# Optimization experiments

Hardware: AMD Instinct MI355X
Metric: run time of the kernel (lower is better)

## Reference

```python
import jax, jax.numpy as jnp
import numpy as np

NUM_HEADS = 16
D_MODEL = 1024
HEAD_DIM = D_MODEL // NUM_HEADS
EMB = 1024
B, L = 2, 2048


def setup_inputs() -> dict:
    key = jax.random.key(0)
    k1, k2, k3 = jax.random.split(key, 3)
    scale_in = 1.0 / np.sqrt(EMB)
    scale_out = 1.0 / np.sqrt(D_MODEL)
    return {
        "x": jax.random.normal(k1, (B, L, EMB), dtype=jnp.float32),
        "W_qkv": jax.random.normal(k2, (EMB, 3 * D_MODEL), dtype=jnp.float32) * scale_in,
        "b_qkv": jnp.zeros((3 * D_MODEL,), dtype=jnp.float32),
        "W_out": jax.random.normal(k3, (D_MODEL, EMB), dtype=jnp.float32) * scale_out,
        "b_out": jnp.zeros((EMB,), dtype=jnp.float32),
    }


def reference(x, W_qkv, b_qkv, W_out, b_out):
    Bn, Ln, _ = x.shape
    qkv = x @ W_qkv + b_qkv  # [B, L, 3*d_model]
    q = qkv[:, :, :D_MODEL].reshape(Bn, Ln, NUM_HEADS, HEAD_DIM)
    k = qkv[:, :, D_MODEL:2 * D_MODEL].reshape(Bn, Ln, NUM_HEADS, HEAD_DIM)
    v = qkv[:, :, 2 * D_MODEL:].reshape(Bn, Ln, NUM_HEADS, HEAD_DIM)
    scores = jnp.einsum('bqhd,bkhd->bhqk', q, k)  # [B, H, L, L]
    attn = jax.nn.softmax(scores / jnp.sqrt(jnp.float32(HEAD_DIM)), axis=-1)
    out = jnp.einsum('bhqk,bkhd->bqhd', attn, v).reshape(Bn, Ln, D_MODEL)
    return out @ W_out + b_out
```

## Files before the change

kernel.cpp:

```cpp
#include <hip/hip_runtime.h>
#include <stdint.h>

#define B_   2
#define L_   2048
#define H_   16
#define D_   64
#define EMB_ 1024
#define DM_  1024
#define N3_  3072
#define TOK_ 4096

typedef unsigned short u16;
typedef unsigned int u32;
typedef __attribute__((ext_vector_type(4))) float f32x4;
typedef __attribute__((ext_vector_type(8))) short s16x8;
typedef __attribute__((ext_vector_type(4))) u32 u32x4;
typedef __attribute__((ext_vector_type(2))) u32 u32x2;
typedef __attribute__((ext_vector_type(4))) u16 u16x4;

#define MFMA(a,b,c) __builtin_amdgcn_mfma_f32_16x16x32_bf16(a,b,c,0,0,0)

#define AS1 __attribute__((address_space(1)))
#define AS3 __attribute__((address_space(3)))
#define GLLDS(g, l) __builtin_amdgcn_global_load_lds( \
    (const AS1 u32*)(const void*)(g), (AS3 u32*)(void*)(l), 16, 0, 0)

#define QSCALE 0.18033688011f

static __device__ __forceinline__ u16 f2bf(float f) {
  u32 u = __builtin_bit_cast(u32, f);
  u = (u + 0x7fffu + ((u >> 16) & 1u)) >> 16;
  return (u16)u;
}

static __device__ __forceinline__ u32 pack2bf(float a, float b) {
#if __has_builtin(__builtin_amdgcn_cvt_pk_bf16_f32)
  auto v = __builtin_amdgcn_cvt_pk_bf16_f32(a, b);
  return __builtin_bit_cast(u32, v);
#else
  return (u32)f2bf(a) | ((u32)f2bf(b) << 16);
#endif
}

static __device__ __forceinline__ float fexp2(float x) {
#if __has_builtin(__builtin_amdgcn_exp2f)
  return __builtin_amdgcn_exp2f(x);
#else
  float r;
  asm("v_exp_f32 %0, %1" : "=v"(r) : "v"(x));
  return r;
#endif
}

__global__ __launch_bounds__(256) void k_prep(
    const float* __restrict__ x,   u16* __restrict__ xb,
    const float* __restrict__ Wq,  u16* __restrict__ wqT,
    const float* __restrict__ Wo,  u16* __restrict__ woT)
{
  const int blk = blockIdx.x, tid = threadIdx.x;
  if (blk < 4096) {
    int i = (blk * 256 + tid) * 4;
    float4 v = *(const float4*)(x + i);
    ushort4 o;
    o.x = f2bf(v.x); o.y = f2bf(v.y); o.z = f2bf(v.z); o.w = f2bf(v.w);
    *(ushort4*)(xb + i) = o;
    return;
  }
  __shared__ float tile[32][33];
  const float* in;
  u16* out;
  int R, C, bx, by;
  if (blk < 4096 + 3072) {
    int t = blk - 4096;
    in = Wq; out = wqT; R = EMB_; C = N3_;
    bx = t % 96; by = t / 96;
  } else {
    int t = blk - 7168;
    in = Wo; out = woT; R = DM_; C = DM_;
    bx = t & 31; by = t >> 5;
  }
  int c0 = bx * 32, r0 = by * 32;
  int tx = tid & 31, ty = tid >> 5;
  #pragma unroll
  for (int i = 0; i < 32; i += 8)
    tile[ty + i][tx] = in[(size_t)(r0 + ty + i) * C + (c0 + tx)];
  __syncthreads();
  #pragma unroll
  for (int i = 0; i < 32; i += 8)
    out[(size_t)(c0 + ty + i) * R + (r0 + tx)] = f2bf(tile[tx][ty + i]);
}

template<int EPI>
__global__ __launch_bounds__(256, 2) void k_gemm(
    const u16* __restrict__ A, const u16* __restrict__ Bt,
    const float* __restrict__ bias, int M, int N, int K,
    float* __restrict__ Cf,
    u16* __restrict__ Qo, u16* __restrict__ Ko, u16* __restrict__ Vo)
{
  const int tid = threadIdx.x;
  const int wave = tid >> 6, lane = tid & 63;
  const int lr = lane & 15, lk = lane >> 4;
  const int wr = wave >> 1, wc = wave & 1;
  const int m0 = blockIdx.y * 128, n0 = blockIdx.x * 128;

  __shared__ u16 As[128 * 32];
  __shared__ u16 Bs[128 * 32];

  f32x4 acc[4][4] = {};

  const int srow = wave * 32 + (lane >> 2);
  const int schunk = (lane & 3) * 8;
  const u16* gA0 = A  + (size_t)(m0 + srow) * K + schunk;
  const u16* gB0 = Bt + (size_t)(n0 + srow) * K + schunk;
  const u16* gA1 = gA0 + (size_t)16 * K;
  const u16* gB1 = gB0 + (size_t)16 * K;
  u16* lA = As + wave * (32 * 32);
  u16* lB = Bs + wave * (32 * 32);

  for (int k0 = 0; k0 < K; k0 += 32) {
    __syncthreads();
    GLLDS(gA0 + k0, lA);
    GLLDS(gA1 + k0, lA + 16 * 32);
    GLLDS(gB0 + k0, lB);
    GLLDS(gB1 + k0, lB + 16 * 32);
    __syncthreads();

    s16x8 af[4], bf[4];
    #pragma unroll
    for (int mi = 0; mi < 4; ++mi)
      af[mi] = *(const s16x8*)(As + (wr * 64 + mi * 16 + lr) * 32 + lk * 8);
    #pragma unroll
    for (int ni = 0; ni < 4; ++ni)
      bf[ni] = *(const s16x8*)(Bs + (wc * 64 + ni * 16 + lr) * 32 + lk * 8);
    #pragma unroll
    for (int mi = 0; mi < 4; ++mi)
      #pragma unroll
      for (int ni = 0; ni < 4; ++ni)
        acc[mi][ni] = MFMA(af[mi], bf[ni], acc[mi][ni]);
  }

  const int mbase = m0 + wr * 64 + lk * 4;
  #pragma unroll
  for (int ni = 0; ni < 4; ++ni) {
    int gn = n0 + wc * 64 + ni * 16 + lr;
    float bz = bias[gn];
    #pragma unroll
    for (int mi = 0; mi < 4; ++mi) {
      #pragma unroll
      for (int r = 0; r < 4; ++r) {
        int gm = mbase + mi * 16 + r;
        float v = acc[mi][ni][r] + bz;
        if (EPI == 1) {
          Cf[(size_t)gm * N + gn] = v;
        } else {
          int sec = gn >> 10, cm = gn & 1023;
          int h = cm >> 6, d = cm & 63;
          int b = gm >> 11, l = gm & 2047;
          int bh = b * H_ + h;
          if (sec == 0)      Qo[((size_t)bh * L_ + l) * D_ + d] = f2bf(v * QSCALE);
          else if (sec == 1) Ko[((size_t)bh * L_ + l) * D_ + d] = f2bf(v);
          else               Vo[((size_t)bh * D_ + d) * L_ + l] = f2bf(v);
        }
      }
    }
  }
}

__global__ __launch_bounds__(256, 2) void k_flash(
    const u16* __restrict__ Q, const u16* __restrict__ Kb,
    const u16* __restrict__ Vt, u16* __restrict__ AO)
{
  const int tid = threadIdx.x;
  const int wave = tid >> 6, lane = tid & 63;
  const int lr = lane & 15, lk = lane >> 4;
  const int blk = blockIdx.x;
  const int idx = blk >> 3;
  const int bh = (blk & 7) * 4 + (idx >> 4);
  const int qt = idx & 15;
  const int b = bh >> 4, h = bh & 15;
  const u16* Qh = Q  + (size_t)bh * L_ * D_;
  const u16* Kh = Kb + (size_t)bh * L_ * D_;
  const u16* Vh = Vt + (size_t)bh * D_ * L_;

  __shared__ u16 Ks[2][64 * 64];
  __shared__ u16 Vs[2][64 * 64];
  __shared__ u16 Ps[128 * 64];

  const int qrow0 = qt * 128 + wave * 32;
  s16x8 qf[2][2];
  #pragma unroll
  for (int g = 0; g < 2; ++g)
    #pragma unroll
    for (int ks = 0; ks < 2; ++ks)
      qf[g][ks] = *(const s16x8*)(Qh + (size_t)(qrow0 + g * 16 + lr) * D_ + ks * 32 + lk * 8);

  f32x4 acco[2][4] = {};
  float lst[2] = {0.f, 0.f};

  const int srow0 = wave * 16 + (lane >> 3);
  const int gch8 = (((lane & 7) ^ ((lane >> 3) & 7)) * 8);
  u16* kd0 = (u16*)Ks[0] + wave * (16 * 64);
  u16* kd1 = (u16*)Ks[1] + wave * (16 * 64);
  u16* vd0 = (u16*)Vs[0] + wave * (16 * 64);
  u16* vd1 = (u16*)Vs[1] + wave * (16 * 64);

  const int ck0 = (lk ^ (lr & 7)) * 8;
  const int sxor = (lr & 7) << 1;
  u16* PsW = Ps + wave * (32 * 64);

  GLLDS(Kh + (size_t)srow0 * 64 + gch8,        kd0);
  GLLDS(Kh + (size_t)(srow0 + 8) * 64 + gch8,  kd0 + 8 * 64);
  GLLDS(Vh + (size_t)srow0 * L_ + gch8,        vd0);
  GLLDS(Vh + (size_t)(srow0 + 8) * L_ + gch8,  vd0 + 8 * 64);

  int buf = 0;
  for (int t0 = 0; t0 < L_; t0 += 64, buf ^= 1) {
    __syncthreads();

    if (t0 + 64 < L_) {
      const int tn = t0 + 64;
      u16* kd = buf ? kd0 : kd1;
      u16* vd = buf ? vd0 : vd1;
      GLLDS(Kh + (size_t)(tn + srow0) * 64 + gch8,       kd);
      GLLDS(Kh + (size_t)(tn + srow0 + 8) * 64 + gch8,   kd + 8 * 64);
      GLLDS(Vh + ((size_t)srow0 * L_ + tn + gch8),       vd);
      GLLDS(Vh + ((size_t)(srow0 + 8) * L_ + tn + gch8), vd + 8 * 64);
    }

    const u16* Kbuf = (const u16*)Ks[buf];
    f32x4 accs[2][4] = {};
    s16x8 kf[4][2];
    #pragma unroll
    for (int mi = 0; mi < 4; ++mi) {
      const u16* rp = Kbuf + (mi * 16 + lr) * 64;
      kf[mi][0] = *(const s16x8*)(rp + ck0);
      kf[mi][1] = *(const s16x8*)(rp + (ck0 ^ 32));
    }
    #pragma unroll
    for (int mi = 0; mi < 4; ++mi)
      #pragma unroll
      for (int g = 0; g < 2; ++g) {
        accs[g][mi] = MFMA(kf[mi][0], qf[g][0], accs[g][mi]);
        accs[g][mi] = MFMA(kf[mi][1], qf[g][1], accs[g][mi]);
      }

    #pragma unroll
    for (int g = 0; g < 2; ++g) {
      const int prow = (g * 16 + lr) * 64;
      #pragma unroll
      for (int mi = 0; mi < 4; ++mi) {
        float p0 = fexp2(accs[g][mi][0]);
        float p1 = fexp2(accs[g][mi][1]);
        float p2 = fexp2(accs[g][mi][2]);
        float p3 = fexp2(accs[g][mi][3]);
        lst[g] += (p0 + p1) + (p2 + p3);
        u32x2 pk = { pack2bf(p0, p1), pack2bf(p2, p3) };
        *(u32x2*)(PsW + prow + (((4 * mi + lk) ^ sxor) * 4)) = pk;
      }
    }

    const u16* Vbuf = (const u16*)Vs[buf];
    s16x8 vf[4][2], pf[2][2];
    #pragma unroll
    for (int di = 0; di < 4; ++di) {
      const u16* rp = Vbuf + (di * 16 + lr) * 64;
      vf[di][0] = *(const s16x8*)(rp + ck0);
      vf[di][1] = *(const s16x8*)(rp + (ck0 ^ 32));
    }
    #pragma unroll
    for (int g = 0; g < 2; ++g) {
      const int prow = (g * 16 + lr) * 64;
      pf[g][0] = *(const s16x8*)(PsW + prow + (((2 * lk) ^ sxor) * 4));
      pf[g][1] = *(const s16x8*)(PsW + prow + (((8 + 2 * lk) ^ sxor) * 4));
    }
    #pragma unroll
    for (int di = 0; di < 4; ++di)
      #pragma unroll
      for (int g = 0; g < 2; ++g) {
        acco[g][di] = MFMA(vf[di][0], pf[g][0], acco[g][di]);
        acco[g][di] = MFMA(vf[di][1], pf[g][1], acco[g][di]);
      }
  }

  #pragma unroll
  for (int g = 0; g < 2; ++g) {
    float l = lst[g];
    l += __shfl_xor(l, 16);
    l += __shfl_xor(l, 32);
    float rl = 1.0f / l;
    const int q = qrow0 + g * 16 + lr;
    #pragma unroll
    for (int di = 0; di < 4; ++di) {
      u16x4 o;
      #pragma unroll
      for (int r = 0; r < 4; ++r)
        o[r] = f2bf(acco[g][di][r] * rl);
      *(u16x4*)(AO + (size_t)(b * L_ + q) * DM_ + h * D_ + di * 16 + lk * 4) = o;
    }
  }
}

extern "C" void kernel_launch(void* const* d_in, const int* in_sizes, int n_in,
                              void* d_out, int out_size, void* d_ws, size_t ws_size,
                              hipStream_t stream)
{
  const float* x    = (const float*)d_in[0];
  const float* Wqkv = (const float*)d_in[1];
  const float* bqkv = (const float*)d_in[2];
  const float* Wout = (const float*)d_in[3];
  const float* bout = (const float*)d_in[4];
  float* out = (float*)d_out;

  u16* xb  = (u16*)d_ws;
  u16* wqT = xb  + (size_t)TOK_ * EMB_;
  u16* woT = wqT + (size_t)N3_ * EMB_;
  u16* qb  = woT + (size_t)DM_ * EMB_;
  u16* kb  = qb  + (size_t)B_ * H_ * L_ * D_;
  u16* vt  = kb  + (size_t)B_ * H_ * L_ * D_;
  u16* ao  = vt  + (size_t)B_ * H_ * L_ * D_;

  k_prep<<<4096 + 3072 + 1024, 256, 0, stream>>>(x, xb, Wqkv, wqT, Wout, woT);
  k_gemm<0><<<dim3(N3_ / 128, TOK_ / 128), 256, 0, stream>>>(
      xb, wqT, bqkv, TOK_, N3_, EMB_, nullptr, qb, kb, vt);
  k_flash<<<512, 256, 0, stream>>>(qb, kb, vt, ao);
  k_gemm<1><<<dim3(DM_ / 128, TOK_ / 128), 256, 0, stream>>>(
      ao, woT, bout, TOK_, DM_, EMB_, out, nullptr, nullptr, nullptr);
}
```

Measured before the change: 198.7 us.

## Double-buffer GEMM LDS tiles and vectorize V-transpose epilogue stores

The GEMM main loop now uses two LDS buffers per operand. The next K-slice is issued via global_load_lds before the MFMAs on the current slice, which removes one of the two barriers per iteration and aims to overlap global loads with compute. The QKV epilogue also writes the transposed V section as 4-element vector stores along L instead of scalar stores. LDS use doubles to 32KB per block, which may affect occupancy at 2 blocks per CU. Correctness depends on the async LDS loads completing before the barrier, since waitcnt placement is implicit.

Result: faster. 193.2 us (-2.8%).

```diff
diff --git a/kernel.cpp b/kernel.cpp
--- a/kernel.cpp
+++ b/kernel.cpp
@@ -103,35 +103,48 @@
   const int wr = wave >> 1, wc = wave & 1;
   const int m0 = blockIdx.y * 128, n0 = blockIdx.x * 128;
 
-  __shared__ u16 As[128 * 32];
-  __shared__ u16 Bs[128 * 32];
+  __shared__ u16 As[2][128 * 32];
+  __shared__ u16 Bs[2][128 * 32];
 
   f32x4 acc[4][4] = {};
 
   const int srow = wave * 32 + (lane >> 2);
   const int schunk = (lane & 3) * 8;
-  const u16* gA0 = A  + (size_t)(m0 + srow) * K + schunk;
-  const u16* gB0 = Bt + (size_t)(n0 + srow) * K + schunk;
-  const u16* gA1 = gA0 + (size_t)16 * K;
-  const u16* gB1 = gB0 + (size_t)16 * K;
-  u16* lA = As + wave * (32 * 32);
-  u16* lB = Bs + wave * (32 * 32);
-
-  for (int k0 = 0; k0 < K; k0 += 32) {
+  const u16* gA = A  + (size_t)(m0 + srow) * K + schunk;
+  const u16* gB = Bt + (size_t)(n0 + srow) * K + schunk;
+  const size_t rstep = (size_t)16 * K;
+  u16* lA0 = (u16*)As[0] + wave * (32 * 32);
+  u16* lA1 = (u16*)As[1] + wave * (32 * 32);
+  u16* lB0 = (u16*)Bs[0] + wave * (32 * 32);
+  u16* lB1 = (u16*)Bs[1] + wave * (32 * 32);
+
+  GLLDS(gA,         lA0);
+  GLLDS(gA + rstep, lA0 + 16 * 32);
+  GLLDS(gB,         lB0);
+  GLLDS(gB + rstep, lB0 + 16 * 32);
+
+  int buf = 0;
+  for (int k0 = 0; k0 < K; k0 += 32, buf ^= 1) {
     __syncthreads();
-    GLLDS(gA0 + k0, lA);
-    GLLDS(gA1 + k0, lA + 16 * 32);
-    GLLDS(gB0 + k0, lB);
-    GLLDS(gB1 + k0, lB + 16 * 32);
-    __syncthreads();
-
+
+    if (k0 + 32 < K) {
+      u16* dA = buf ? lA0 : lA1;
+      u16* dB = buf ? lB0 : lB1;
+      GLLDS(gA + k0 + 32,         dA);
+      GLLDS(gA + k0 + 32 + rstep, dA + 16 * 32);
+      GLLDS(gB + k0 + 32,         dB);
+      GLLDS(gB + k0 + 32 + rstep, dB + 16 * 32);
+    }
+
+    const u16* Ab = (const u16*)As[buf];
+    const u16* Bb = (const u16*)Bs[buf];
     s16x8 af[4], bf[4];
     #pragma unroll
     for (int mi = 0; mi < 4; ++mi)
-      af[mi] = *(const s16x8*)(As + (wr * 64 + mi * 16 + lr) * 32 + lk * 8);
+      af[mi] = *(const s16x8*)(Ab + (wr * 64 + mi * 16 + lr) * 32 + lk * 8);
     #pragma unroll
     for (int ni = 0; ni < 4; ++ni)
-      bf[ni] = *(const s16x8*)(Bs + (wc * 64 + ni * 16 + lr) * 32 + lk * 8);
+      bf[ni] = *(const s16x8*)(Bb + (wc * 64 + ni * 16 + lr) * 32 + lk * 8);
     #pragma unroll
     for (int mi = 0; mi < 4; ++mi)
       #pragma unroll
@@ -144,23 +157,40 @@
   for (int ni = 0; ni < 4; ++ni) {
     int gn = n0 + wc * 64 + ni * 16 + lr;
     float bz = bias[gn];
-    #pragma unroll
-    for (int mi = 0; mi < 4; ++mi) {
-      #pragma unroll
-      for (int r = 0; r < 4; ++r) {
-        int gm = mbase + mi * 16 + r;
-        float v = acc[mi][ni][r] + bz;
-        if (EPI == 1) {
-          Cf[(size_t)gm * N + gn] = v;
-        } else {
-          int sec = gn >> 10, cm = gn & 1023;
-          int h = cm >> 6, d = cm & 63;
-          int b = gm >> 11, l = gm & 2047;
+    if (EPI == 1) {
+      #pragma unroll
+      for (int mi = 0; mi < 4; ++mi)
+        #pragma unroll
+        for (int r = 0; r < 4; ++r) {
+          int gm = mbase + mi * 16 + r;
+          Cf[(size_t)gm * N + gn] = acc[mi][ni][r] + bz;
+        }
+    } else {
+      int sec = gn >> 10, cm = gn & 1023;
+      int h = cm >> 6, d = cm & 63;
+      if (sec == 2) {
+        #pragma unroll
+        for (int mi = 0; mi < 4; ++mi) {
+          int gm0 = mbase + mi * 16;
+          int b = gm0 >> 11, l0 = gm0 & 2047;
           int bh = b * H_ + h;
-          if (sec == 0)      Qo[((size_t)bh * L_ + l) * D_ + d] = f2bf(v * QSCALE);
-          else if (sec == 1) Ko[((size_t)bh * L_ + l) * D_ + d] = f2bf(v);
-          else               Vo[((size_t)bh * D_ + d) * L_ + l] = f2bf(v);
+          u16x4 vv;
+          #pragma unroll
+          for (int r = 0; r < 4; ++r) vv[r] = f2bf(acc[mi][ni][r] + bz);
+          *(u16x4*)(Vo + ((size_t)bh * D_ + d) * L_ + l0) = vv;
         }
+      } else {
+        #pragma unroll
+        for (int mi = 0; mi < 4; ++mi)
+          #pragma unroll
+          for (int r = 0; r < 4; ++r) {
+            int gm = mbase + mi * 16 + r;
+            float v = acc[mi][ni][r] + bz;
+            int b = gm >> 11, l = gm & 2047;
+            int bh = b * H_ + h;
+            if (sec == 0) Qo[((size_t)bh * L_ + l) * D_ + d] = f2bf(v * QSCALE);
+            else          Ko[((size_t)bh * L_ + l) * D_ + d] = f2bf(v);
+          }
       }
     }
   }
```
